# Kernel tuning notes

Hardware: AMD Instinct MI355X
Metric: run time of the kernel (lower is better)

## Reference

```python
import jax, jax.numpy as jnp
import numpy as np

NUM_EMBEDDINGS = 512
EMBEDDING_DIM = 128
COMMITMENT_COST = 0.25


def setup_inputs() -> dict:
    key = jax.random.key(0)
    k1, k2 = jax.random.split(key)
    inputs = jax.random.normal(k1, (8, EMBEDDING_DIM, 32, 32, 32), dtype=jnp.float32)
    limit = 1.0 / NUM_EMBEDDINGS
    weight = jax.random.uniform(k2, (NUM_EMBEDDINGS, EMBEDDING_DIM), dtype=jnp.float32,
                                minval=-limit, maxval=limit)
    return {"inputs": inputs, "weight": weight}


def reference(inputs, weight):
    sg = jax.lax.stop_gradient
    # (B, C, D, H, W) -> (B, D, H, W, C)
    x = jnp.transpose(inputs, (0, 2, 3, 4, 1))
    C = x.shape[-1]
    flat = x.reshape(-1, C)  # [N, C]
    distances = (jnp.sum(flat * flat, axis=1, keepdims=True)
                 + jnp.sum(weight * weight, axis=1)
                 - 2.0 * flat @ weight.T)
    encoding_indices = jnp.argmin(distances, axis=1)  # [N]
    encodings = jax.nn.one_hot(encoding_indices, weight.shape[0], dtype=jnp.float32)  # [N, E]
    # gather is mathematically identical to encodings @ weight
    quantized = weight[encoding_indices].reshape(x.shape)
    e_latent_loss = jnp.mean((sg(quantized) - x) ** 2)
    q_latent_loss = jnp.mean((quantized - sg(x)) ** 2)
    loss = q_latent_loss + COMMITMENT_COST * e_latent_loss
    # straight-through estimator
    quantized_st = x + sg(quantized - x)
    avg_probs = jnp.mean(encodings, axis=0)
    perplexity = jnp.exp(-jnp.sum(avg_probs * jnp.log(avg_probs + 1e-10)))
    out_q = jnp.transpose(quantized_st, (0, 4, 1, 2, 3))  # back to (B, C, D, H, W)
    return loss, out_q, perplexity, encodings
```

## Files before the change

kernel.cpp:

```cpp
#include <hip/hip_runtime.h>
#include <math.h>

#define CDIM 128
#define EDIM 512
#define BLK 256
#define MT 128
#define NCH 128
#define KCH 32
#define NVEC 262144
#define SPATIAL 32768
#define QELEMS 33554432LL

struct WS {
  float  wnh[EDIM];
  int    counts[EDIM];
  double lossAcc;
  double _pad;
  float  wT[CDIM * EDIM];
};

__global__ __launch_bounds__(512) void vq_pre(const float* __restrict__ wt,
                                              WS* __restrict__ ws, int buildWT) {
  int t = threadIdx.x;
  const float* w = wt + (size_t)t * CDIM;
  float a0 = 0.f, a1 = 0.f, a2 = 0.f, a3 = 0.f;
#pragma unroll
  for (int c = 0; c < CDIM; c += 4) {
    a0 = fmaf(w[c + 0], w[c + 0], a0);
    a1 = fmaf(w[c + 1], w[c + 1], a1);
    a2 = fmaf(w[c + 2], w[c + 2], a2);
    a3 = fmaf(w[c + 3], w[c + 3], a3);
  }
  ws->wnh[t] = 0.5f * ((a0 + a1) + (a2 + a3));
  ws->counts[t] = 0;
  if (t == 0) ws->lossAcc = 0.0;
  if (buildWT) {
    for (int c = 0; c < CDIM; ++c) ws->wT[c * EDIM + t] = w[c];
  }
}

__device__ double score64(const float* __restrict__ in, const float* __restrict__ wt,
                          size_t xoff, int e) {
  const float* w = wt + (size_t)e * CDIM;
  double a = 0.0;
  for (int c = 0; c < CDIM; ++c) {
    double wd = (double)w[c];
    double xv = (double)in[xoff + (size_t)c * SPATIAL];
    a = fma(wd, fma(0.5, wd, -xv), a);
  }
  return a;
}

template <bool USEWT>
__global__ __launch_bounds__(BLK, 3) void vq_main(const float* __restrict__ in,
                                                  const float* __restrict__ wt,
                                                  WS* __restrict__ ws,
                                                  float* __restrict__ out_q,
                                                  float* __restrict__ enc) {
  __shared__ __align__(16) char uni[43520];
  float (*xt)[MT]  = (float(*)[MT])uni;
  float (*wl)[NCH] = (float(*)[NCH])(uni + KCH * MT * 4);
  float (*cb1)[17] = (float(*)[17])uni;
  float (*cb2)[17] = (float(*)[17])(uni + 8704);
  float (*cb3)[17] = (float(*)[17])(uni + 17408);
  int   (*ci1)[17] = (int(*)[17])(uni + 26112);
  int   (*ci2)[17] = (int(*)[17])(uni + 34816);
  __shared__ float  wn_l[EDIM];
  __shared__ int    hist[EDIM];
  __shared__ int    sIdx[MT];
  __shared__ double lred[BLK];

  const int tid = threadIdx.x;
  for (int e = tid; e < EDIM; e += BLK) { wn_l[e] = ws->wnh[e]; hist[e] = 0; }

  const int n0 = blockIdx.x * MT;
  const int b  = n0 >> 15;
  const int s0 = n0 & (SPATIAL - 1);
  const size_t ibase = (size_t)b * CDIM * SPATIAL;

  const int tm = tid & 15, tn = tid >> 4;
  const int sg = tid & 31, sk = tid >> 5;
  const int wq8 = tid & 7, wn32 = tid >> 3;

  float acc[8][8];
  float bst1[8], bst2[8], bst3[8];
  int   bi1[8], bi2[8];
#pragma unroll
  for (int i = 0; i < 8; ++i) { bst1[i] = 1e30f; bst2[i] = 1e30f; bst3[i] = 1e30f; bi1[i] = 0; bi2[i] = 0; }

  for (int nc = 0; nc < EDIM / NCH; ++nc) {
#pragma unroll
    for (int i = 0; i < 8; ++i)
#pragma unroll
      for (int j = 0; j < 8; ++j) acc[i][j] = 0.f;

    for (int kc = 0; kc < CDIM / KCH; ++kc) {
      __syncthreads();
#pragma unroll
      for (int p = 0; p < 4; ++p) {
        int k = sk + 8 * p;
        float4 v = *(const float4*)(in + ibase + (size_t)(kc * KCH + k) * SPATIAL + s0 + sg * 4);
        *(float4*)&xt[k][sg * 4] = v;
      }
      if (USEWT) {
#pragma unroll
        for (int p = 0; p < 4; ++p) {
          int k = sk + 8 * p;
          float4 v = *(const float4*)(ws->wT + (size_t)(kc * KCH + k) * EDIM + nc * NCH + sg * 4);
          *(float4*)&wl[k][sg * 4] = v;
        }
      } else {
#pragma unroll
        for (int p = 0; p < 4; ++p) {
          int nn = wn32 + 32 * p;
          float4 v = *(const float4*)(wt + (size_t)(nc * NCH + nn) * CDIM + kc * KCH + wq8 * 4);
          wl[wq8 * 4 + 0][nn] = v.x; wl[wq8 * 4 + 1][nn] = v.y;
          wl[wq8 * 4 + 2][nn] = v.z; wl[wq8 * 4 + 3][nn] = v.w;
        }
      }
      __syncthreads();
#pragma unroll 2
      for (int k = 0; k < KCH; ++k) {
        float4 xa = *(const float4*)&xt[k][tm * 8];
        float4 xb = *(const float4*)&xt[k][tm * 8 + 4];
        float4 wa = *(const float4*)&wl[k][tn * 8];
        float4 wb = *(const float4*)&wl[k][tn * 8 + 4];
        float xf[8] = {xa.x, xa.y, xa.z, xa.w, xb.x, xb.y, xb.z, xb.w};
        float wf[8] = {wa.x, wa.y, wa.z, wa.w, wb.x, wb.y, wb.z, wb.w};
#pragma unroll
        for (int i = 0; i < 8; ++i)
#pragma unroll
          for (int j = 0; j < 8; ++j) acc[i][j] = fmaf(xf[i], wf[j], acc[i][j]);
      }
    }
#pragma unroll
    for (int j = 0; j < 8; ++j) {
      int e = nc * NCH + tn * 8 + j;
      float wn = wn_l[e];
#pragma unroll
      for (int i = 0; i < 8; ++i) {
        float sc = wn - acc[i][j];
        if (sc < bst1[i]) { bst3[i] = bst2[i]; bst2[i] = bst1[i]; bi2[i] = bi1[i]; bst1[i] = sc; bi1[i] = e; }
        else if (sc < bst2[i]) { bst3[i] = bst2[i]; bst2[i] = sc; bi2[i] = e; }
        else if (sc < bst3[i]) { bst3[i] = sc; }
      }
    }
  }

  __syncthreads();
#pragma unroll
  for (int i = 0; i < 8; ++i) {
    int vec = tm * 8 + i;
    cb1[vec][tn] = bst1[i]; cb2[vec][tn] = bst2[i]; cb3[vec][tn] = bst3[i];
    ci1[vec][tn] = bi1[i];  ci2[vec][tn] = bi2[i];
  }
  __syncthreads();

  if (tid < MT) {
    const int vec = tid;
    float m1 = 1e30f, m2 = 1e30f, m3 = 1e30f;
    int j1 = 0x7fffffff, j2 = 0x7fffffff;
    auto ins = [&](float v, int ix) {
      bool b1 = (v < m1) || (v == m1 && ix < j1);
      bool b2 = (v < m2) || (v == m2 && ix < j2);
      if (b1)      { m3 = m2; m2 = m1; j2 = j1; m1 = v; j1 = ix; }
      else if (b2) { m3 = m2; m2 = v; j2 = ix; }
      else if (v < m3) { m3 = v; }
    };
    for (int t = 0; t < 16; ++t) {
      ins(cb1[vec][t], ci1[vec][t]);
      ins(cb2[vec][t], ci2[vec][t]);
      ins(cb3[vec][t], 0x7fffffff);
    }
    int bi = j1;
    const size_t xoff = ibase + s0 + vec;
    if (m3 - m1 < 2e-6f) {
      double bd = 1e300; int bj = 0;
      for (int e = 0; e < EDIM; ++e) {
        double a = score64(in, wt, xoff, e);
        if (a < bd) { bd = a; bj = e; }
      }
      bi = bj;
    } else if (m2 - m1 < 2e-6f) {
      double s1 = score64(in, wt, xoff, j1);
      double s2 = score64(in, wt, xoff, j2);
      if (s2 < s1 || (s2 == s1 && j2 < j1)) bi = j2;
    }
    sIdx[vec] = bi;
    atomicAdd(&hist[bi], 1);
  }
  __syncthreads();

  {
    const int vec = tid & (MT - 1);
    const int half = tid >> 7;
    const int bi = sIdx[vec];
    const float* wq2 = wt + (size_t)bi * CDIM;
    const size_t base = ibase + s0 + vec;
    double ls = 0.0;
#pragma unroll 4
    for (int c = half * 64; c < half * 64 + 64; ++c) {
      float xv = in[base + (size_t)c * SPATIAL];
      float qv = wq2[c];
      out_q[base + (size_t)c * SPATIAL] = qv;
      double d = (double)qv - (double)xv;
      ls = fma(d, d, ls);
    }
    lred[tid] = ls;
  }
  __syncthreads();
  for (int off = BLK / 2; off > 0; off >>= 1) {
    if (tid < off) lred[tid] += lred[tid + off];
    __syncthreads();
  }
  if (tid == 0) atomicAdd(&ws->lossAcc, lred[0]);

  {
    float2* e2 = (float2*)enc;
    const size_t r0 = (size_t)blockIdx.x * MT;
    const int c0 = tid * 2;
    for (int r = 0; r < MT; ++r) {
      int idx = sIdx[r];
      float2 v;
      v.x = (idx == c0) ? 1.0f : 0.0f;
      v.y = (idx == c0 + 1) ? 1.0f : 0.0f;
      e2[(r0 + (size_t)r) * (EDIM / 2) + tid] = v;
    }
  }

  for (int e = tid; e < EDIM; e += BLK) {
    int v = hist[e];
    if (v) atomicAdd(&ws->counts[e], v);
  }
}

__global__ __launch_bounds__(512) void vq_fin(const WS* __restrict__ ws, float* __restrict__ out) {
  __shared__ double red[EDIM];
  int t = threadIdx.x;
  double p = (double)ws->counts[t] * (1.0 / (double)NVEC);
  red[t] = p * log(p + 1e-10);
  __syncthreads();
  for (int off = 256; off > 0; off >>= 1) {
    if (t < off) red[t] += red[t + off];
    __syncthreads();
  }
  if (t == 0) {
    out[0] = (float)(1.25 * ws->lossAcc / (double)QELEMS);
    out[1 + QELEMS] = (float)exp(-red[0]);
  }
}

extern "C" void kernel_launch(void* const* d_in, const int* in_sizes, int n_in,
                              void* d_out, int out_size, void* d_ws, size_t ws_size,
                              hipStream_t stream) {
  const float* in = (const float*)d_in[0];
  const float* wt = (const float*)d_in[1];
  float* out = (float*)d_out;
  WS* ws = (WS*)d_ws;

  float* out_q = out + 1;
  float* enc   = out + 2 + QELEMS;

  const bool useWT = (ws_size >= sizeof(WS));
  vq_pre<<<dim3(1), dim3(512), 0, stream>>>(wt, ws, useWT ? 1 : 0);
  if (useWT)
    vq_main<true><<<dim3(NVEC / MT), dim3(BLK), 0, stream>>>(in, wt, ws, out_q, enc);
  else
    vq_main<false><<<dim3(NVEC / MT), dim3(BLK), 0, stream>>>(in, wt, ws, out_q, enc);
  vq_fin<<<dim3(1), dim3(512), 0, stream>>>(ws, out);
}
```

Baseline: 1.139 ms.

## Compute VQ distances with split-bf16 MFMA instead of FP32 FMA tiles

Replaces the scalar FP32 register-tiled distance GEMM with bf16 MFMA 16x16x32 instructions. Both the inputs and the codebook are split into hi and lo bf16 parts, and three-to-four products are accumulated to approximate FP32 accuracy. The codebook is pre-packed as hi/lo pairs in the workspace. The tile shrinks to 64 vectors per block, and the loss now reuses the x values cached in LDS instead of re-reading global memory. Outputs use nontemporal stores. The tie threshold is widened to cover the extra bf16 error, which may send more vectors down the slow fp64 fallback.

```diff
diff --git a/kernel.cpp b/kernel.cpp
--- a/kernel.cpp
+++ b/kernel.cpp
@@ -4,23 +4,34 @@
 #define CDIM 128
 #define EDIM 512
 #define BLK 256
-#define MT 128
-#define NCH 128
-#define KCH 32
+#define MT 64
+#define ECH 64
 #define NVEC 262144
 #define SPATIAL 32768
 #define QELEMS 33554432LL
+#define TIE_T 4e-6f
+
+typedef __bf16 bf16x8 __attribute__((ext_vector_type(8)));
+typedef float  f32x4  __attribute__((ext_vector_type(4)));
 
 struct WS {
   float  wnh[EDIM];
   int    counts[EDIM];
   double lossAcc;
   double _pad;
-  float  wT[CDIM * EDIM];
+  unsigned int wp[EDIM * CDIM];
 };
 
+__device__ inline unsigned short f2bf(float f) {
+  unsigned u = __float_as_uint(f);
+  return (unsigned short)((u + 0x7fffu + ((u >> 16) & 1u)) >> 16);
+}
+__device__ inline float bf2f(unsigned short h) {
+  return __uint_as_float(((unsigned)h) << 16);
+}
+
 __global__ __launch_bounds__(512) void vq_pre(const float* __restrict__ wt,
-                                              WS* __restrict__ ws, int buildWT) {
+                                              WS* __restrict__ ws, int buildWP) {
   int t = threadIdx.x;
   const float* w = wt + (size_t)t * CDIM;
   float a0 = 0.f, a1 = 0.f, a2 = 0.f, a3 = 0.f;
@@ -34,8 +45,13 @@
   ws->wnh[t] = 0.5f * ((a0 + a1) + (a2 + a3));
   ws->counts[t] = 0;
   if (t == 0) ws->lossAcc = 0.0;
-  if (buildWT) {
-    for (int c = 0; c < CDIM; ++c) ws->wT[c * EDIM + t] = w[c];
+  if (buildWP) {
+    for (int c = 0; c < CDIM; ++c) {
+      float f = w[c];
+      unsigned short h = f2bf(f);
+      unsigned short l = f2bf(f - bf2f(h));
+      ws->wp[(size_t)t * CDIM + c] = (((unsigned)h) << 16) | (unsigned)l;
+    }
   }
 }
 
@@ -51,25 +67,24 @@
   return a;
 }
 
-template <bool USEWT>
-__global__ __launch_bounds__(BLK, 3) void vq_main(const float* __restrict__ in,
+
+template <bool USEWP>
+__global__ __launch_bounds__(BLK, 2) void vq_main(const float* __restrict__ in,
                                                   const float* __restrict__ wt,
                                                   WS* __restrict__ ws,
                                                   float* __restrict__ out_q,
                                                   float* __restrict__ enc) {
-  __shared__ __align__(16) char uni[43520];
-  float (*xt)[MT]  = (float(*)[MT])uni;
-  float (*wl)[NCH] = (float(*)[NCH])(uni + KCH * MT * 4);
-  float (*cb1)[17] = (float(*)[17])uni;
-  float (*cb2)[17] = (float(*)[17])(uni + 8704);
-  float (*cb3)[17] = (float(*)[17])(uni + 17408);
-  int   (*ci1)[17] = (int(*)[17])(uni + 26112);
-  int   (*ci2)[17] = (int(*)[17])(uni + 34816);
+  __shared__ __align__(16) unsigned short xhi[4 * 2176];
+  __shared__ __align__(16) unsigned short xlo[4 * 2176];
+  __shared__ __align__(16) char wuni[2 * ECH * 136 * 2];
   __shared__ float  wn_l[EDIM];
   __shared__ int    hist[EDIM];
   __shared__ int    sIdx[MT];
   __shared__ double lred[BLK];
 
+  unsigned short* whl = (unsigned short*)wuni;
+  unsigned short* wll = whl + ECH * 136;
+
   const int tid = threadIdx.x;
   for (int e = tid; e < EDIM; e += BLK) { wn_l[e] = ws->wnh[e]; hist[e] = 0; }
 
@@ -78,81 +93,120 @@
   const int s0 = n0 & (SPATIAL - 1);
   const size_t ibase = (size_t)b * CDIM * SPATIAL;
 
-  const int tm = tid & 15, tn = tid >> 4;
-  const int sg = tid & 31, sk = tid >> 5;
-  const int wq8 = tid & 7, wn32 = tid >> 3;
-
-  float acc[8][8];
-  float bst1[8], bst2[8], bst3[8];
-  int   bi1[8], bi2[8];
-#pragma unroll
-  for (int i = 0; i < 8; ++i) { bst1[i] = 1e30f; bst2[i] = 1e30f; bst3[i] = 1e30f; bi1[i] = 0; bi2[i] = 0; }
-
-  for (int nc = 0; nc < EDIM / NCH; ++nc) {
-#pragma unroll
-    for (int i = 0; i < 8; ++i)
-#pragma unroll
-      for (int j = 0; j < 8; ++j) acc[i][j] = 0.f;
-
-    for (int kc = 0; kc < CDIM / KCH; ++kc) {
-      __syncthreads();
-#pragma unroll
-      for (int p = 0; p < 4; ++p) {
-        int k = sk + 8 * p;
-        float4 v = *(const float4*)(in + ibase + (size_t)(kc * KCH + k) * SPATIAL + s0 + sg * 4);
-        *(float4*)&xt[k][sg * 4] = v;
-      }
-      if (USEWT) {
-#pragma unroll
-        for (int p = 0; p < 4; ++p) {
-          int k = sk + 8 * p;
-          float4 v = *(const float4*)(ws->wT + (size_t)(kc * KCH + k) * EDIM + nc * NCH + sg * 4);
-          *(float4*)&wl[k][sg * 4] = v;
-        }
-      } else {
-#pragma unroll
-        for (int p = 0; p < 4; ++p) {
-          int nn = wn32 + 32 * p;
-          float4 v = *(const float4*)(wt + (size_t)(nc * NCH + nn) * CDIM + kc * KCH + wq8 * 4);
-          wl[wq8 * 4 + 0][nn] = v.x; wl[wq8 * 4 + 1][nn] = v.y;
-          wl[wq8 * 4 + 2][nn] = v.z; wl[wq8 * 4 + 3][nn] = v.w;
-        }
-      }
-      __syncthreads();
-#pragma unroll 2
-      for (int k = 0; k < KCH; ++k) {
-        float4 xa = *(const float4*)&xt[k][tm * 8];
-        float4 xb = *(const float4*)&xt[k][tm * 8 + 4];
-        float4 wa = *(const float4*)&wl[k][tn * 8];
-        float4 wb = *(const float4*)&wl[k][tn * 8 + 4];
-        float xf[8] = {xa.x, xa.y, xa.z, xa.w, xb.x, xb.y, xb.z, xb.w};
-        float wf[8] = {wa.x, wa.y, wa.z, wa.w, wb.x, wb.y, wb.z, wb.w};
-#pragma unroll
-        for (int i = 0; i < 8; ++i)
-#pragma unroll
-          for (int j = 0; j < 8; ++j) acc[i][j] = fmaf(xf[i], wf[j], acc[i][j]);
-      }
-    }
-#pragma unroll
-    for (int j = 0; j < 8; ++j) {
-      int e = nc * NCH + tn * 8 + j;
-      float wn = wn_l[e];
+  {
+    const int mq = tid & 15;
+    const int cr = tid >> 4;
+    const int m0 = mq * 4;
+#pragma unroll
+    for (int p = 0; p < 8; ++p) {
+      int c = cr + p * 16;
+      float4 v = *(const float4*)(in + ibase + (size_t)c * SPATIAL + s0 + m0);
+      int sb = (m0 >> 4) * 2176 + (c >> 3) * 136 + (m0 & 15) * 8 + (c & 7);
+#pragma unroll
+      for (int i = 0; i < 4; ++i) {
+        float f = ((const float*)&v)[i];
+        unsigned short h = f2bf(f);
+        unsigned short l = f2bf(f - bf2f(h));
+        xhi[sb + i * 8] = h;
+        xlo[sb + i * 8] = l;
+      }
+    }
+  }
+
+  const int lane = tid & 63, wv = tid >> 6;
+  const int col = lane & 15, g = lane >> 4;
+
+  float b1[4], b2[4], b3[4]; int i1[4], i2[4];
+#pragma unroll
+  for (int i = 0; i < 4; ++i) { b1[i] = 1e30f; b2[i] = 1e30f; b3[i] = 1e30f; i1[i] = 0; i2[i] = 0; }
+
+  for (int ch = 0; ch < 8; ++ch) {
+    const int e0c = ch * ECH;
+    __syncthreads();
+    if (USEWP) {
+      const uint4* wp4 = (const uint4*)(ws->wp + (size_t)e0c * CDIM);
 #pragma unroll
       for (int i = 0; i < 8; ++i) {
-        float sc = wn - acc[i][j];
-        if (sc < bst1[i]) { bst3[i] = bst2[i]; bst2[i] = bst1[i]; bi2[i] = bi1[i]; bst1[i] = sc; bi1[i] = e; }
-        else if (sc < bst2[i]) { bst3[i] = bst2[i]; bst2[i] = sc; bi2[i] = e; }
-        else if (sc < bst3[i]) { bst3[i] = sc; }
-      }
-    }
-  }
-
-  __syncthreads();
-#pragma unroll
-  for (int i = 0; i < 8; ++i) {
-    int vec = tm * 8 + i;
-    cb1[vec][tn] = bst1[i]; cb2[vec][tn] = bst2[i]; cb3[vec][tn] = bst3[i];
-    ci1[vec][tn] = bi1[i];  ci2[vec][tn] = bi2[i];
+        int q = i * BLK + tid;
+        int e = q >> 5, k0 = (q & 31) * 4;
+        uint4 W = wp4[q];
+        unsigned hi01 = __builtin_amdgcn_perm(W.y, W.x, 0x07060302u);
+        unsigned lo01 = __builtin_amdgcn_perm(W.y, W.x, 0x05040100u);
+        unsigned hi23 = __builtin_amdgcn_perm(W.w, W.z, 0x07060302u);
+        unsigned lo23 = __builtin_amdgcn_perm(W.w, W.z, 0x05040100u);
+        *(uint2*)&whl[e * 136 + k0] = make_uint2(hi01, hi23);
+        *(uint2*)&wll[e * 136 + k0] = make_uint2(lo01, lo23);
+      }
+    } else {
+      const float* wbase = wt + (size_t)e0c * CDIM;
+#pragma unroll
+      for (int i = 0; i < 8; ++i) {
+        int q = i * BLK + tid;
+        int e = q >> 5, k0 = (q & 31) * 4;
+        float4 F = *(const float4*)(wbase + (size_t)e * CDIM + k0);
+        unsigned short h0 = f2bf(F.x), h1 = f2bf(F.y), h2 = f2bf(F.z), h3 = f2bf(F.w);
+        unsigned short l0 = f2bf(F.x - bf2f(h0)), l1 = f2bf(F.y - bf2f(h1));
+        unsigned short l2 = f2bf(F.z - bf2f(h2)), l3 = f2bf(F.w - bf2f(h3));
+        *(uint2*)&whl[e * 136 + k0] =
+            make_uint2((unsigned)h0 | ((unsigned)h1 << 16), (unsigned)h2 | ((unsigned)h3 << 16));
+        *(uint2*)&wll[e * 136 + k0] =
+            make_uint2((unsigned)l0 | ((unsigned)l1 << 16), (unsigned)l2 | ((unsigned)l3 << 16));
+      }
+    }
+    __syncthreads();
+
+    bf16x8 ah[4], al[4];
+#pragma unroll
+    for (int kt = 0; kt < 4; ++kt) {
+      int rowb = (wv * 16 + col) * 136 + kt * 32 + g * 8;
+      ah[kt] = *(const bf16x8*)&whl[rowb];
+      al[kt] = *(const bf16x8*)&wll[rowb];
+    }
+
+    f32x4 acc[4];
+#pragma unroll
+    for (int mt = 0; mt < 4; ++mt) {
+      f32x4 a = {0.f, 0.f, 0.f, 0.f};
+#pragma unroll
+      for (int kt = 0; kt < 4; ++kt) {
+        int xb = mt * 2176 + (kt * 4 + g) * 136 + col * 8;
+        bf16x8 bh = *(const bf16x8*)&xhi[xb];
+        bf16x8 bl = *(const bf16x8*)&xlo[xb];
+        a = __builtin_amdgcn_mfma_f32_16x16x32_bf16(ah[kt], bh, a, 0, 0, 0);
+        a = __builtin_amdgcn_mfma_f32_16x16x32_bf16(ah[kt], bl, a, 0, 0, 0);
+        a = __builtin_amdgcn_mfma_f32_16x16x32_bf16(al[kt], bh, a, 0, 0, 0);
+        a = __builtin_amdgcn_mfma_f32_16x16x32_bf16(al[kt], bl, a, 0, 0, 0);
+      }
+      acc[mt] = a;
+    }
+
+    const int e0 = e0c + wv * 16 + g * 4;
+    float4 wn = *(const float4*)&wn_l[e0];
+#pragma unroll
+    for (int mt = 0; mt < 4; ++mt) {
+#pragma unroll
+      for (int r = 0; r < 4; ++r) {
+        float sc = ((const float*)&wn)[r] - acc[mt][r];
+        int e = e0 + r;
+        if (sc < b1[mt]) { b3[mt] = b2[mt]; b2[mt] = b1[mt]; i2[mt] = i1[mt]; b1[mt] = sc; i1[mt] = e; }
+        else if (sc < b2[mt]) { b3[mt] = b2[mt]; b2[mt] = sc; i2[mt] = e; }
+        else if (sc < b3[mt]) { b3[mt] = sc; }
+      }
+    }
+  }
+
+  __syncthreads();
+  float (*cb1)[17] = (float(*)[17])wuni;
+  float (*cb2)[17] = (float(*)[17])(wuni + 4352);
+  float (*cb3)[17] = (float(*)[17])(wuni + 8704);
+  int   (*ci1)[17] = (int(*)[17])(wuni + 13056);
+  int   (*ci2)[17] = (int(*)[17])(wuni + 17408);
+
+#pragma unroll
+  for (int mt = 0; mt < 4; ++mt) {
+    int m = mt * 16 + col, slot = wv * 4 + g;
+    cb1[m][slot] = b1[mt]; cb2[m][slot] = b2[mt]; cb3[m][slot] = b3[mt];
+    ci1[m][slot] = i1[mt]; ci2[m][slot] = i2[mt];
   }
   __syncthreads();
 
@@ -161,10 +215,10 @@
     float m1 = 1e30f, m2 = 1e30f, m3 = 1e30f;
     int j1 = 0x7fffffff, j2 = 0x7fffffff;
     auto ins = [&](float v, int ix) {
-      bool b1 = (v < m1) || (v == m1 && ix < j1);
-      bool b2 = (v < m2) || (v == m2 && ix < j2);
-      if (b1)      { m3 = m2; m2 = m1; j2 = j1; m1 = v; j1 = ix; }
-      else if (b2) { m3 = m2; m2 = v; j2 = ix; }
+      bool q1 = (v < m1) || (v == m1 && ix < j1);
+      bool q2 = (v < m2) || (v == m2 && ix < j2);
+      if (q1)      { m3 = m2; m2 = m1; j2 = j1; m1 = v; j1 = ix; }
+      else if (q2) { m3 = m2; m2 = v; j2 = ix; }
       else if (v < m3) { m3 = v; }
     };
     for (int t = 0; t < 16; ++t) {
@@ -174,14 +228,14 @@
     }
     int bi = j1;
     const size_t xoff = ibase + s0 + vec;
-    if (m3 - m1 < 2e-6f) {
+    if (m3 - m1 < TIE_T) {
       double bd = 1e300; int bj = 0;
       for (int e = 0; e < EDIM; ++e) {
         double a = score64(in, wt, xoff, e);
         if (a < bd) { bd = a; bj = e; }
       }
       bi = bj;
-    } else if (m2 - m1 < 2e-6f) {
+    } else if (m2 - m1 < TIE_T) {
       double s1 = score64(in, wt, xoff, j1);
       double s2 = score64(in, wt, xoff, j2);
       if (s2 < s1 || (s2 == s1 && j2 < j1)) bi = j2;
@@ -193,18 +247,30 @@
 
   {
     const int vec = tid & (MT - 1);
-    const int half = tid >> 7;
-    const int bi = sIdx[vec];
-    const float* wq2 = wt + (size_t)bi * CDIM;
-    const size_t base = ibase + s0 + vec;
+    const int qd  = tid >> 6;
+    const int bi  = sIdx[vec];
+    const float* wq = wt + (size_t)bi * CDIM;
+    const size_t gbase = ibase + s0 + vec;
     double ls = 0.0;
-#pragma unroll 4
-    for (int c = half * 64; c < half * 64 + 64; ++c) {
-      float xv = in[base + (size_t)c * SPATIAL];
-      float qv = wq2[c];
-      out_q[base + (size_t)c * SPATIAL] = qv;
-      double d = (double)qv - (double)xv;
-      ls = fma(d, d, ls);
+#pragma unroll
+    for (int cc = 0; cc < 32; cc += 4) {
+      int c = qd * 32 + cc;
+      int eb = (vec >> 4) * 2176 + (c >> 3) * 136 + (vec & 15) * 8 + (c & 7);
+      uint2 hq = *(const uint2*)&xhi[eb];
+      uint2 lq = *(const uint2*)&xlo[eb];
+      float xs0 = bf2f((unsigned short)(hq.x & 0xffffu)) + bf2f((unsigned short)(lq.x & 0xffffu));
+      float xs1 = bf2f((unsigned short)(hq.x >> 16))     + bf2f((unsigned short)(lq.x >> 16));
+      float xs2 = bf2f((unsigned short)(hq.y & 0xffffu)) + bf2f((unsigned short)(lq.y & 0xffffu));
+      float xs3 = bf2f((unsigned short)(hq.y >> 16))     + bf2f((unsigned short)(lq.y >> 16));
+      float4 qv = *(const float4*)(wq + c);
+      __builtin_nontemporal_store(qv.x, out_q + gbase + (size_t)(c + 0) * SPATIAL);
+      __builtin_nontemporal_store(qv.y, out_q + gbase + (size_t)(c + 1) * SPATIAL);
+      __builtin_nontemporal_store(qv.z, out_q + gbase + (size_t)(c + 2) * SPATIAL);
+      __builtin_nontemporal_store(qv.w, out_q + gbase + (size_t)(c + 3) * SPATIAL);
+      double d0 = (double)qv.x - (double)xs0; ls = fma(d0, d0, ls);
+      double d1 = (double)qv.y - (double)xs1; ls = fma(d1, d1, ls);
+      double d2 = (double)qv.z - (double)xs2; ls = fma(d2, d2, ls);
+      double d3 = (double)qv.w - (double)xs3; ls = fma(d3, d3, ls);
     }
     lred[tid] = ls;
   }
@@ -216,15 +282,15 @@
   if (tid == 0) atomicAdd(&ws->lossAcc, lred[0]);
 
   {
-    float2* e2 = (float2*)enc;
     const size_t r0 = (size_t)blockIdx.x * MT;
     const int c0 = tid * 2;
+    unsigned long long* e2 = (unsigned long long*)enc;
     for (int r = 0; r < MT; ++r) {
       int idx = sIdx[r];
-      float2 v;
-      v.x = (idx == c0) ? 1.0f : 0.0f;
-      v.y = (idx == c0 + 1) ? 1.0f : 0.0f;
-      e2[(r0 + (size_t)r) * (EDIM / 2) + tid] = v;
+      union { float2 f; unsigned long long u; } cvt;
+      cvt.f.x = (idx == c0) ? 1.0f : 0.0f;
+      cvt.f.y = (idx == c0 + 1) ? 1.0f : 0.0f;
+      __builtin_nontemporal_store(cvt.u, e2 + (r0 + (size_t)r) * (EDIM / 2) + tid);
     }
   }
 
@@ -261,9 +327,9 @@
   float* out_q = out + 1;
   float* enc   = out + 2 + QELEMS;
 
-  const bool useWT = (ws_size >= sizeof(WS));
-  vq_pre<<<dim3(1), dim3(512), 0, stream>>>(wt, ws, useWT ? 1 : 0);
-  if (useWT)
+  const bool useWP = (ws_size >= sizeof(WS));
+  vq_pre<<<dim3(1), dim3(512), 0, stream>>>(wt, ws, useWP ? 1 : 0);
+  if (useWP)
     vq_main<true><<<dim3(NVEC / MT), dim3(BLK), 0, stream>>>(in, wt, ws, out_q, enc);
   else
     vq_main<false><<<dim3(NVEC / MT), dim3(BLK), 0, stream>>>(in, wt, ws, out_q, enc);
```

New measurement: 1.045 ms. -8.3%, faster.
